# Performance work log

Hardware: AMD Instinct MI355X
Metric: run time of the kernel (lower is better)

Reference implementation:

```python
import jax, jax.numpy as jnp
import numpy as np
from jax import lax

B, C, H, W = 2, 512, 128, 128
HEADS = 4


def conv1x1(x, w):
    # x: [b,c,h,w], w: [o,c] (1x1 conv kernel squeezed)
    return jnp.einsum('bchw,oc->bohw', x, w)


def dwconv3x3(x, w):
    # depthwise 3x3, SAME padding; w: [c,1,3,3]
    return lax.conv_general_dilated(
        x, w, window_strides=(1, 1), padding='SAME',
        dimension_numbers=('NCHW', 'OIHW', 'NCHW'),
        feature_group_count=x.shape[1])


def l2norm(t):
    # F.normalize(dim=-1): x / max(||x||_2, eps)
    n = jnp.sqrt(jnp.sum(t * t, axis=-1, keepdims=True))
    return t / jnp.maximum(n, 1e-12)


def setup_inputs() -> dict:
    key = jax.random.key(0)
    ks = jax.random.split(key, 10)
    s = 0.02
    return {
        'x': jax.random.normal(ks[0], (B, C, H, W), jnp.float32),
        'y': jax.random.normal(ks[1], (B, C, H, W), jnp.float32),
        'temperature': jnp.ones((HEADS, 1, 1), jnp.float32),
        'q_w': s * jax.random.normal(ks[2], (C, C), jnp.float32),
        'q_dw': s * jax.random.normal(ks[3], (C, 1, 3, 3), jnp.float32),
        'kv_w': s * jax.random.normal(ks[4], (2 * C, C), jnp.float32),
        'kv_dw': s * jax.random.normal(ks[5], (2 * C, 1, 3, 3), jnp.float32),
        'proj_w': s * jax.random.normal(ks[6], (C, C), jnp.float32),
        'pos_embed': jnp.zeros((1, C, 1, 1), jnp.float32),
        'pos_q_w': s * jax.random.normal(ks[7], (C, C), jnp.float32),
        'pos_k_w': s * jax.random.normal(ks[8], (C, C), jnp.float32),
    }


def reference(x, y, temperature, q_w, q_dw, kv_w, kv_dw, proj_w, pos_embed, pos_q_w, pos_k_w):
    b, c, h, w = x.shape
    heads = temperature.shape[0]
    ch = c // heads

    def to_heads(t):  # [b,c,h,w] -> [b,head,ch,hw]
        return t.reshape(b, heads, ch, h * w)

    q = dwconv3x3(conv1x1(x, q_w), q_dw)
    kv = dwconv3x3(conv1x1(y, kv_w), kv_dw)
    k, v = jnp.split(kv, 2, axis=1)

    qh = l2norm(to_heads(q))
    kh = l2norm(to_heads(k))
    vh = to_heads(v)

    attn = jax.nn.softmax(jnp.einsum('bhcn,bhdn->bhcd', qh, kh) * temperature, axis=-1)
    out = jnp.einsum('bhcd,bhdn->bhcn', attn, vh)

    pos_x = x + pos_embed
    pq = to_heads(conv1x1(pos_x, pos_q_w))
    pk = to_heads(conv1x1(pos_x, pos_k_w))
    pos_attn = jax.nn.softmax(jnp.einsum('bhcn,bhdn->bhcd', pq, pk), axis=-1)
    pos_out = jnp.einsum('bhcd,bhdn->bhcn', pos_attn, vh)

    fused = (out + pos_out).reshape(b, c, h, w)
    return conv1x1(fused, proj_w)
```

## Files before the change

### kernel.cpp

```cpp
#include <hip/hip_runtime.h>


typedef _Float16 f16_t;
typedef __attribute__((ext_vector_type(8))) _Float16 f16x8;
typedef __attribute__((ext_vector_type(4))) float f32x4;

#define NDIM 16384

__device__ __forceinline__ void gload_lds16(const void* g, void* l) {
  __builtin_amdgcn_global_load_lds((__attribute__((address_space(1))) void*)g,
                                   (__attribute__((address_space(3))) void*)l, 16, 0, 0);
}

template<int EPI>
__device__ __forceinline__ void gemm_core_128(
    const f16_t* __restrict__ At, int lda,
    const f16_t* __restrict__ Bt, int ldb,
    void* __restrict__ Ct, int ldc, int K)
{
  __shared__ f16_t As[128 * 32];
  __shared__ f16_t Bs[128 * 32];
  const int tid = threadIdx.x;
  const int lane = tid & 63;
  const int wave = tid >> 6;
  const int wm = (wave >> 1) * 64;
  const int wn = (wave & 1) * 64;
  const int lr = lane & 15;
  const int lq = lane >> 4;

  const f16_t* gA0 = At + (size_t)(tid >> 2) * lda + (tid & 3) * 8;
  const f16_t* gA1 = At + (size_t)((tid + 256) >> 2) * lda + (tid & 3) * 8;
  const f16_t* gB0 = Bt + (size_t)(tid >> 2) * ldb + (tid & 3) * 8;
  const f16_t* gB1 = Bt + (size_t)((tid + 256) >> 2) * ldb + (tid & 3) * 8;
  f16_t* lA0 = &As[tid * 8];
  f16_t* lA1 = &As[(tid + 256) * 8];
  f16_t* lB0 = &Bs[tid * 8];
  f16_t* lB1 = &Bs[(tid + 256) * 8];

  f32x4 acc[4][4] = {};

  for (int kk = 0; kk < K; kk += 32) {
    if (kk) __syncthreads();
    gload_lds16(gA0 + kk, lA0);
    gload_lds16(gA1 + kk, lA1);
    gload_lds16(gB0 + kk, lB0);
    gload_lds16(gB1 + kk, lB1);
    __syncthreads();

    f16x8 af[4], bfr[4];
#pragma unroll
    for (int i = 0; i < 4; i++) {
      af[i]  = *(const f16x8*)&As[(wm + i * 16 + lr) * 32 + lq * 8];
      bfr[i] = *(const f16x8*)&Bs[(wn + i * 16 + lr) * 32 + lq * 8];
    }
#pragma unroll
    for (int i = 0; i < 4; i++)
#pragma unroll
      for (int j = 0; j < 4; j++)
        acc[i][j] = __builtin_amdgcn_mfma_f32_16x16x32_f16(af[i], bfr[j], acc[i][j], 0, 0, 0);
  }

#pragma unroll
  for (int i = 0; i < 4; i++)
#pragma unroll
    for (int j = 0; j < 4; j++)
#pragma unroll
      for (int r = 0; r < 4; r++) {
        int row = wm + i * 16 + lq * 4 + r;
        int col = wn + j * 16 + lr;
        float v = acc[i][j][r];
        if (EPI == 0)      ((f16_t*)Ct)[(size_t)row * ldc + col] = (f16_t)v;
        else if (EPI == 1) ((float*)Ct)[(size_t)row * ldc + col] = v;
        else               atomicAdd(&((float*)Ct)[(size_t)row * ldc + col], v);
      }
}

template<int EPI, typename CT>
__global__ __launch_bounds__(256) void gemm_bt_kernel(
    const f16_t* __restrict__ A, int lda, const f16_t* __restrict__ B, int ldb,
    CT* __restrict__ C, int ldc, int K)
{
  const f16_t* At = A + (size_t)blockIdx.y * 128 * lda;
  const f16_t* Bt = B + (size_t)blockIdx.x * 128 * ldb;
  CT* Ct = C + (size_t)blockIdx.y * 128 * ldc + (size_t)blockIdx.x * 128;
  gemm_core_128<EPI>(At, lda, Bt, ldb, (void*)Ct, ldc, K);
}

__global__ __launch_bounds__(256) void gram_kernel(
    const f16_t* __restrict__ xc, float* __restrict__ Gb)
{
  int ks = blockIdx.x, t = blockIdx.y;
  int ty = t >> 2, tx = t & 3;
  const f16_t* At = xc + (size_t)ty * 128 * NDIM + ks * 1024;
  const f16_t* Bt = xc + (size_t)tx * 128 * NDIM + ks * 1024;
  float* Ct = Gb + (size_t)ty * 128 * 512 + tx * 128;
  gemm_core_128<2>(At, NDIM, Bt, NDIM, Ct, 512, 1024);
}

__global__ __launch_bounds__(256) void qk_kernel(
    const f16_t* __restrict__ q, const f16_t* __restrict__ k,
    float* __restrict__ lgs_b)
{
  int ks = blockIdx.x, h = blockIdx.y;
  const f16_t* At = q + (size_t)h * 128 * NDIM + ks * 512;
  const f16_t* Bt = k + (size_t)h * 128 * NDIM + ks * 512;
  float* Ct = lgs_b + (size_t)h * 16384;
  gemm_core_128<2>(At, NDIM, Bt, NDIM, Ct, 128, 512);
}

__global__ __launch_bounds__(256) void transpose2_kernel(
    const float* __restrict__ sx, const float* __restrict__ sy,
    f16_t* __restrict__ dx, f16_t* __restrict__ dy)
{
  const float* src = blockIdx.z ? sy : sx;
  f16_t* dst = blockIdx.z ? dy : dx;
  __shared__ f16_t tile[32][33];
  int tx = threadIdx.x & 31, ty = threadIdx.x >> 5;
  int r0 = blockIdx.y * 32, c0 = blockIdx.x * 32;
#pragma unroll
  for (int k = 0; k < 4; k++) {
    int r = ty + k * 8;
    tile[r][tx] = (f16_t)src[(size_t)(r0 + r) * NDIM + c0 + tx];
  }
  __syncthreads();
#pragma unroll
  for (int k = 0; k < 4; k++) {
    int r = ty + k * 8;
    dst[(size_t)(c0 + r) * 512 + r0 + tx] = tile[tx][r];
  }
}

__global__ __launch_bounds__(256) void transpose_f16_kernel(
    const f16_t* __restrict__ src, f16_t* __restrict__ dst)
{
  __shared__ f16_t tile[32][33];
  int tx = threadIdx.x & 31, ty = threadIdx.x >> 5;
  int r0 = blockIdx.y * 32, c0 = blockIdx.x * 32;
#pragma unroll
  for (int k = 0; k < 4; k++) {
    int r = ty + k * 8;
    tile[r][tx] = src[(size_t)(r0 + r) * NDIM + c0 + tx];
  }
  __syncthreads();
#pragma unroll
  for (int k = 0; k < 4; k++) {
    int r = ty + k * 8;
    dst[(size_t)(c0 + r) * 512 + r0 + tx] = tile[tx][r];
  }
}

__global__ __launch_bounds__(256) void cast_x_kernel(
    const float* __restrict__ xb, f16_t* __restrict__ xc, float* __restrict__ srow_b)
{
  int c = blockIdx.y;
  int n = blockIdx.x * 256 + threadIdx.x;
  float v = xb[(size_t)c * NDIM + n];
  xc[(size_t)c * NDIM + n] = (f16_t)v;
  __shared__ float red[256];
  red[threadIdx.x] = v;
  __syncthreads();
  for (int s = 128; s > 0; s >>= 1) {
    if (threadIdx.x < s) red[threadIdx.x] += red[threadIdx.x + s];
    __syncthreads();
  }
  if (threadIdx.x == 0) atomicAdd(&srow_b[c], red[0]);
}

__global__ __launch_bounds__(256) void dwconv_kernel(
    const f16_t* __restrict__ in, const float* __restrict__ w,
    f16_t* __restrict__ outA, f16_t* __restrict__ outB,
    int splitC, float* __restrict__ norm2)
{
  const int c = blockIdx.y;
  const int t = threadIdx.x;
  const int xs = (t & 15) * 8;
  const int h0 = blockIdx.x * 64 + (t >> 4) * 4;
  const f16_t* src = in + (size_t)c * NDIM;
  const float* wc = w + c * 9;
  float w00 = wc[0], w01 = wc[1], w02 = wc[2];
  float w10 = wc[3], w11 = wc[4], w12 = wc[5];
  float w20 = wc[6], w21 = wc[7], w22 = wc[8];

  float rows[6][10];
#pragma unroll
  for (int i = 0; i < 6; i++) {
    int hh = h0 - 1 + i;
    int hc = hh < 0 ? 0 : (hh > 127 ? 127 : hh);
    f16x8 v = *(const f16x8*)(src + hc * 128 + xs);
    float l = __shfl_up((float)v[7], 1, 64);
    float r = __shfl_down((float)v[0], 1, 64);
    if ((t & 15) == 0) l = 0.f;
    if ((t & 15) == 15) r = 0.f;
    bool oob = (hh < 0) || (hh > 127);
    rows[i][0] = oob ? 0.f : l;
    rows[i][9] = oob ? 0.f : r;
#pragma unroll
    for (int j = 0; j < 8; j++) rows[i][1 + j] = oob ? 0.f : (float)v[j];
  }

  float s2 = 0.f;
  f16_t* dst = (c < splitC) ? outA + (size_t)c * NDIM
                            : outB + (size_t)(c - splitC) * NDIM;
#pragma unroll
  for (int i = 0; i < 4; i++) {
    f16x8 o;
#pragma unroll
    for (int j = 0; j < 8; j++) {
      float a = w00 * rows[i][j]     + w01 * rows[i][j + 1]     + w02 * rows[i][j + 2]
              + w10 * rows[i + 1][j] + w11 * rows[i + 1][j + 1] + w12 * rows[i + 1][j + 2]
              + w20 * rows[i + 2][j] + w21 * rows[i + 2][j + 1] + w22 * rows[i + 2][j + 2];
      o[j] = (f16_t)a;
      s2 += a * a;
    }
    *(f16x8*)(dst + (h0 + i) * 128 + xs) = o;
  }

  if (c < splitC) {
    __shared__ float red[256];
    red[t] = s2;
    __syncthreads();
    for (int s = 128; s > 0; s >>= 1) {
      if (t < s) red[t] += red[t + s];
      __syncthreads();
    }
    if (t == 0) atomicAdd(&norm2[c], red[0]);
  }
}

__global__ __launch_bounds__(64) void vec4_kernel(
    const float* __restrict__ pqw, const float* __restrict__ pkw,
    const float* __restrict__ pe, const float* __restrict__ srow_b,
    float* __restrict__ bq, float* __restrict__ bk,
    float* __restrict__ tq_b, float* __restrict__ tk_b)
{
  int o = blockIdx.x, which = blockIdx.y, lane = threadIdx.x;
  const float* w = ((which & 1) == 0) ? pqw + (size_t)o * 512 : pkw + (size_t)o * 512;
  const float* v = (which < 2) ? pe : srow_b;
  float s = 0.f;
  for (int c = lane; c < 512; c += 64) s += w[c] * v[c];
#pragma unroll
  for (int off = 32; off > 0; off >>= 1) s += __shfl_down(s, off, 64);
  if (lane == 0) {
    float* dst = (which == 0) ? bq : (which == 1) ? bk : (which == 2) ? tq_b : tk_b;
    dst[o] = s;
  }
}

__global__ __launch_bounds__(256) void posA_kernel(
    const float* __restrict__ pqw, const float* __restrict__ Gb,
    float* __restrict__ PqG)
{
  int tx = threadIdx.x & 15, ty = threadIdx.x >> 4;
  int h = blockIdx.z;
  int r = blockIdx.y * 16 + ty;
  int d = blockIdx.x * 16 + tx;
  const float* wr = pqw + (size_t)(h * 128 + r) * 512;
  float s = 0.f;
#pragma unroll 4
  for (int c = 0; c < 512; c++) s += wr[c] * Gb[(size_t)c * 512 + d];
  PqG[((size_t)h * 128 + r) * 512 + d] = s;
}

__global__ __launch_bounds__(256) void posB_kernel(
    const float* __restrict__ PqG, const float* __restrict__ pkw,
    const float* __restrict__ bq, const float* __restrict__ bk,
    const float* __restrict__ tq_b, const float* __restrict__ tk_b,
    float* __restrict__ lgp)
{
  int tx = threadIdx.x & 15, ty = threadIdx.x >> 4;
  int h = blockIdx.z;
  int r = blockIdx.y * 16 + ty;
  int s = blockIdx.x * 16 + tx;
  int gr = h * 128 + r, gs = h * 128 + s;
  const float* ar = PqG + (size_t)gr * 512;
  const float* kr = pkw + (size_t)gs * 512;
  float acc = 0.f;
#pragma unroll 4
  for (int c = 0; c < 512; c++) acc += ar[c] * kr[c];
  acc += tq_b[gr] * bk[gs] + bq[gr] * tk_b[gs] + 16384.f * bq[gr] * bk[gs];
  lgp[(size_t)h * 16384 + r * 128 + s] = acc;
}

__global__ __launch_bounds__(128) void smx_kernel(
    const float* __restrict__ lgs_b, const float* __restrict__ lgp,
    const float* __restrict__ n2q_b, const float* __restrict__ n2k_b,
    const float* __restrict__ temp, float* __restrict__ comb)
{
  int c = blockIdx.x & 127, h = blockIdx.x >> 7;
  int d = threadIdx.x;
  float rq = fmaxf(sqrtf(n2q_b[h * 128 + c]), 1e-12f);
  float rk = fmaxf(sqrtf(n2k_b[h * 128 + d]), 1e-12f);
  float s0 = lgs_b[(size_t)h * 16384 + c * 128 + d] / (rq * rk) * temp[h];
  float s1 = lgp[(size_t)h * 16384 + c * 128 + d];
  __shared__ float sh[128];
  sh[d] = s0; __syncthreads();
  for (int s = 64; s > 0; s >>= 1) { if (d < s) sh[d] = fmaxf(sh[d], sh[d + s]); __syncthreads(); }
  float m0 = sh[0]; __syncthreads();
  float e0 = __expf(s0 - m0);
  sh[d] = e0; __syncthreads();
  for (int s = 64; s > 0; s >>= 1) { if (d < s) sh[d] += sh[d + s]; __syncthreads(); }
  float z0 = sh[0]; __syncthreads();
  sh[d] = s1; __syncthreads();
  for (int s = 64; s > 0; s >>= 1) { if (d < s) sh[d] = fmaxf(sh[d], sh[d + s]); __syncthreads(); }
  float m1 = sh[0]; __syncthreads();
  float e1 = __expf(s1 - m1);
  sh[d] = e1; __syncthreads();
  for (int s = 64; s > 0; s >>= 1) { if (d < s) sh[d] += sh[d + s]; __syncthreads(); }
  float z1 = sh[0];
  comb[(size_t)h * 16384 + c * 128 + d] = e0 / z0 + e1 / z1;
}

__global__ __launch_bounds__(256) void mb_kernel(
    const float* __restrict__ proj_w, const float* __restrict__ comb,
    f16_t* __restrict__ Mb)
{
  int tx = threadIdx.x & 15, ty = threadIdx.x >> 4;
  int h = blockIdx.z;
  int o = blockIdx.y * 16 + ty;
  int d = blockIdx.x * 16 + tx;
  const float* pw = proj_w + (size_t)o * 512 + h * 128;
  const float* cm = comb + (size_t)h * 16384 + d;
  float s = 0.f;
#pragma unroll 4
  for (int r = 0; r < 128; r++) s += pw[r] * cm[(size_t)r * 128];
  Mb[(size_t)o * 512 + h * 128 + d] = (f16_t)s;
}

__global__ __launch_bounds__(256) void castw_kernel(
    const float* __restrict__ q_w, const float* __restrict__ kv_w,
    f16_t* __restrict__ Wq, f16_t* __restrict__ Wkv)
{
  int i = blockIdx.x * 256 + threadIdx.x;
  if (i < 262144) Wq[i] = (f16_t)q_w[i];
  else Wkv[i - 262144] = (f16_t)kv_w[i - 262144];
}

__global__ __launch_bounds__(256) void zero_kernel(float* __restrict__ p, long n) {
  long i = (long)blockIdx.x * 256 + threadIdx.x;
  if (i < n) p[i] = 0.f;
}

extern "C" void kernel_launch(void* const* d_in, const int* in_sizes, int n_in,
                              void* d_out, int out_size, void* d_ws, size_t ws_size,
                              hipStream_t stream) {
  const float* x      = (const float*)d_in[0];
  const float* y      = (const float*)d_in[1];
  const float* temp   = (const float*)d_in[2];
  const float* q_w    = (const float*)d_in[3];
  const float* q_dw   = (const float*)d_in[4];
  const float* kv_w   = (const float*)d_in[5];
  const float* kv_dw  = (const float*)d_in[6];
  const float* proj_w = (const float*)d_in[7];
  const float* pe     = (const float*)d_in[8];
  const float* pqw    = (const float*)d_in[9];
  const float* pkw    = (const float*)d_in[10];

  const size_t MB = 1ull << 20;
  const size_t N = NDIM;
  char* Wb = (char*)d_ws;
  f16_t* Abuf = (f16_t*)(Wb);
  f16_t* Bbuf = (f16_t*)(Wb + 16 * MB);
  f16_t* Cbuf = (f16_t*)(Wb + 32 * MB);
  f16_t* Dbuf = (f16_t*)(Wb + 48 * MB);
  char* SM = Wb + 64 * MB;
  float* G    = (float*)(SM);
  float* lgs  = (float*)(SM + 2 * MB);
  float* n2q  = (float*)(SM + 2 * MB + 512 * 1024);
  float* n2k  = n2q + 1024;
  float* srow = n2k + 1024;
  float* bq   = (float*)(SM + 3 * MB);
  float* bk   = bq + 512;
  float* tq   = bk + 512;
  float* tk   = tq + 1024;
  f16_t* Wq   = (f16_t*)(SM + 3 * MB + 16 * 1024);
  f16_t* Wkv  = (f16_t*)(SM + 3 * MB + 16 * 1024 + 512 * 1024);
  float* PqG  = (float*)(SM + 5 * MB);
  float* lgp  = (float*)(SM + 6 * MB);
  float* comb = (float*)(SM + 6 * MB + 256 * 1024);
  f16_t* Mb   = (f16_t*)(SM + 6 * MB + 512 * 1024);

  zero_kernel<<<2572, 256, 0, stream>>>((float*)SM, 658432L);
  castw_kernel<<<3072, 256, 0, stream>>>(q_w, kv_w, Wq, Wkv);

  for (int b = 0; b < 2; b++) {
    const float* xb = x + (size_t)b * 512 * N;
    const float* yb = y + (size_t)b * 512 * N;
    float* srow_b = srow + b * 512;
    float* Gb = G + (size_t)b * 512 * 512;
    float* lgs_b = lgs + (size_t)b * 4 * 16384;
    f16_t* kvp = (f16_t*)d_out + (size_t)b * 1024 * N;
    float* outb = (float*)d_out + (size_t)b * 512 * N;

    cast_x_kernel<<<dim3(64, 512), 256, 0, stream>>>(xb, Abuf, srow_b);
    vec4_kernel<<<dim3(512, 4), 64, 0, stream>>>(pqw, pkw, pe, srow_b,
                                                 bq, bk, tq + b * 512, tk + b * 512);
    gram_kernel<<<dim3(16, 16), 256, 0, stream>>>(Abuf, Gb);
    transpose2_kernel<<<dim3(512, 16, 2), 256, 0, stream>>>(xb, yb, Bbuf, Cbuf);
    gemm_bt_kernel<0, f16_t><<<dim3(128, 4), 256, 0, stream>>>(
        Wq, 512, Bbuf, 512, Dbuf, (int)N, 512);
    gemm_bt_kernel<0, f16_t><<<dim3(128, 8), 256, 0, stream>>>(
        Wkv, 512, Cbuf, 512, kvp, (int)N, 512);
    dwconv_kernel<<<dim3(2, 512), 256, 0, stream>>>(
        Dbuf, q_dw, Abuf, (f16_t*)nullptr, 512, n2q + b * 512);
    dwconv_kernel<<<dim3(2, 1024), 256, 0, stream>>>(
        kvp, kv_dw, Dbuf, Cbuf, 512, n2k + b * 512);
    transpose_f16_kernel<<<dim3(512, 16), 256, 0, stream>>>(Cbuf, Bbuf);
    qk_kernel<<<dim3(32, 4), 256, 0, stream>>>(Abuf, Dbuf, lgs_b);
    posA_kernel<<<dim3(32, 8, 4), 256, 0, stream>>>(pqw, Gb, PqG);
    posB_kernel<<<dim3(8, 8, 4), 256, 0, stream>>>(PqG, pkw, bq, bk,
                                                   tq + b * 512, tk + b * 512, lgp);
    smx_kernel<<<512, 128, 0, stream>>>(lgs_b, lgp, n2q + b * 512, n2k + b * 512,
                                        temp, comb);
    mb_kernel<<<dim3(8, 32, 4), 256, 0, stream>>>(proj_w, comb, Mb);
    gemm_bt_kernel<1, float><<<dim3(128, 4), 256, 0, stream>>>(
        Mb, 512, Bbuf, 512, outb, (int)N, 512);
  }

  (void)in_sizes; (void)n_in; (void)out_size; (void)ws_size;
}
```

Measured before the change: 797.3 us.

## Vectorize transposes and cast, use wave-shuffle reductions in cast, dwconv, softmax

The transpose kernels now use 64x64 tiles with 16-byte vector loads and 8-wide f16 vector stores in place of scalar element accesses. The cast kernel handles 8 elements per thread with vector loads and stores. Cast, dwconv and softmax replace LDS tree reductions and their many barriers with wave shuffle reductions. The softmax block shrinks to one wave handling two elements per thread. The aim is to cut memory instruction count and synchronisation overhead in these bandwidth-bound helper kernels, at the risk of LDS bank conflicts in the column reads of the transpose.

After: 658.9 us. -17.4%, faster.

```diff
diff --git a/kernel.cpp b/kernel.cpp
--- a/kernel.cpp
+++ b/kernel.cpp
@@ -2,6 +2,7 @@
 
 
 typedef _Float16 f16_t;
+typedef __attribute__((ext_vector_type(4))) _Float16 f16x4;
 typedef __attribute__((ext_vector_type(8))) _Float16 f16x8;
 typedef __attribute__((ext_vector_type(4))) float f32x4;
 
@@ -114,56 +115,80 @@
 {
   const float* src = blockIdx.z ? sy : sx;
   f16_t* dst = blockIdx.z ? dy : dx;
-  __shared__ f16_t tile[32][33];
-  int tx = threadIdx.x & 31, ty = threadIdx.x >> 5;
-  int r0 = blockIdx.y * 32, c0 = blockIdx.x * 32;
-#pragma unroll
-  for (int k = 0; k < 4; k++) {
-    int r = ty + k * 8;
-    tile[r][tx] = (f16_t)src[(size_t)(r0 + r) * NDIM + c0 + tx];
+  __shared__ f16_t tile[64][72];
+  const int t = threadIdx.x;
+  const int r0 = blockIdx.y * 64, c0 = blockIdx.x * 64;
+  {
+    int tx = t & 15, ty = t >> 4;
+#pragma unroll
+    for (int k = 0; k < 4; k++) {
+      int r = ty + k * 16;
+      f32x4 v = *(const f32x4*)(src + (size_t)(r0 + r) * NDIM + c0 + tx * 4);
+      f16x4 o = { (f16_t)v[0], (f16_t)v[1], (f16_t)v[2], (f16_t)v[3] };
+      *(f16x4*)&tile[r][tx * 4] = o;
+    }
   }
   __syncthreads();
-#pragma unroll
-  for (int k = 0; k < 4; k++) {
-    int r = ty + k * 8;
-    dst[(size_t)(c0 + r) * 512 + r0 + tx] = tile[tx][r];
+  {
+    int j0 = t >> 3, cg = (t & 7) * 8;
+#pragma unroll
+    for (int k = 0; k < 2; k++) {
+      int j = j0 + k * 32;
+      f16x8 o;
+#pragma unroll
+      for (int i = 0; i < 8; i++) o[i] = tile[cg + i][j];
+      *(f16x8*)(dst + (size_t)(c0 + j) * 512 + r0 + cg) = o;
+    }
   }
 }
 
 __global__ __launch_bounds__(256) void transpose_f16_kernel(
     const f16_t* __restrict__ src, f16_t* __restrict__ dst)
 {
-  __shared__ f16_t tile[32][33];
-  int tx = threadIdx.x & 31, ty = threadIdx.x >> 5;
-  int r0 = blockIdx.y * 32, c0 = blockIdx.x * 32;
-#pragma unroll
-  for (int k = 0; k < 4; k++) {
-    int r = ty + k * 8;
-    tile[r][tx] = src[(size_t)(r0 + r) * NDIM + c0 + tx];
+  __shared__ f16_t tile[64][72];
+  const int t = threadIdx.x;
+  const int r0 = blockIdx.y * 64, c0 = blockIdx.x * 64;
+  {
+    int tx = t & 7, ty = t >> 3;
+#pragma unroll
+    for (int k = 0; k < 2; k++) {
+      int r = ty + k * 32;
+      f16x8 v = *(const f16x8*)(src + (size_t)(r0 + r) * NDIM + c0 + tx * 8);
+      *(f16x8*)&tile[r][tx * 8] = v;
+    }
   }
   __syncthreads();
-#pragma unroll
-  for (int k = 0; k < 4; k++) {
-    int r = ty + k * 8;
-    dst[(size_t)(c0 + r) * 512 + r0 + tx] = tile[tx][r];
+  {
+    int j0 = t >> 3, cg = (t & 7) * 8;
+#pragma unroll
+    for (int k = 0; k < 2; k++) {
+      int j = j0 + k * 32;
+      f16x8 o;
+#pragma unroll
+      for (int i = 0; i < 8; i++) o[i] = tile[cg + i][j];
+      *(f16x8*)(dst + (size_t)(c0 + j) * 512 + r0 + cg) = o;
+    }
   }
 }
 
 __global__ __launch_bounds__(256) void cast_x_kernel(
     const float* __restrict__ xb, f16_t* __restrict__ xc, float* __restrict__ srow_b)
 {
-  int c = blockIdx.y;
-  int n = blockIdx.x * 256 + threadIdx.x;
-  float v = xb[(size_t)c * NDIM + n];
-  xc[(size_t)c * NDIM + n] = (f16_t)v;
-  __shared__ float red[256];
-  red[threadIdx.x] = v;
+  const int c = blockIdx.y;
+  const int base = blockIdx.x * 2048 + threadIdx.x * 8;
+  const float* src = xb + (size_t)c * NDIM + base;
+  f32x4 a = *(const f32x4*)src;
+  f32x4 b = *(const f32x4*)(src + 4);
+  f16x8 o = { (f16_t)a[0], (f16_t)a[1], (f16_t)a[2], (f16_t)a[3],
+              (f16_t)b[0], (f16_t)b[1], (f16_t)b[2], (f16_t)b[3] };
+  *(f16x8*)(xc + (size_t)c * NDIM + base) = o;
+  float s = a[0] + a[1] + a[2] + a[3] + b[0] + b[1] + b[2] + b[3];
+#pragma unroll
+  for (int off = 32; off > 0; off >>= 1) s += __shfl_down(s, off, 64);
+  __shared__ float ws[4];
+  if ((threadIdx.x & 63) == 0) ws[threadIdx.x >> 6] = s;
   __syncthreads();
-  for (int s = 128; s > 0; s >>= 1) {
-    if (threadIdx.x < s) red[threadIdx.x] += red[threadIdx.x + s];
-    __syncthreads();
-  }
-  if (threadIdx.x == 0) atomicAdd(&srow_b[c], red[0]);
+  if (threadIdx.x == 0) atomicAdd(&srow_b[c], ws[0] + ws[1] + ws[2] + ws[3]);
 }
 
 __global__ __launch_bounds__(256) void dwconv_kernel(
@@ -216,14 +241,12 @@
   }
 
   if (c < splitC) {
-    __shared__ float red[256];
-    red[t] = s2;
+#pragma unroll
+    for (int off = 32; off > 0; off >>= 1) s2 += __shfl_down(s2, off, 64);
+    __shared__ float ws[4];
+    if ((t & 63) == 0) ws[t >> 6] = s2;
     __syncthreads();
-    for (int s = 128; s > 0; s >>= 1) {
-      if (t < s) red[t] += red[t + s];
-      __syncthreads();
-    }
-    if (t == 0) atomicAdd(&norm2[c], red[0]);
+    if (t == 0) atomicAdd(&norm2[c], ws[0] + ws[1] + ws[2] + ws[3]);
   }
 }
 
@@ -281,33 +304,42 @@
   lgp[(size_t)h * 16384 + r * 128 + s] = acc;
 }
 
-__global__ __launch_bounds__(128) void smx_kernel(
+__global__ __launch_bounds__(64) void smx_kernel(
     const float* __restrict__ lgs_b, const float* __restrict__ lgp,
     const float* __restrict__ n2q_b, const float* __restrict__ n2k_b,
     const float* __restrict__ temp, float* __restrict__ comb)
 {
   int c = blockIdx.x & 127, h = blockIdx.x >> 7;
-  int d = threadIdx.x;
+  int l = threadIdx.x;
+  int d0 = l, d1 = l + 64;
   float rq = fmaxf(sqrtf(n2q_b[h * 128 + c]), 1e-12f);
-  float rk = fmaxf(sqrtf(n2k_b[h * 128 + d]), 1e-12f);
-  float s0 = lgs_b[(size_t)h * 16384 + c * 128 + d] / (rq * rk) * temp[h];
-  float s1 = lgp[(size_t)h * 16384 + c * 128 + d];
-  __shared__ float sh[128];
-  sh[d] = s0; __syncthreads();
-  for (int s = 64; s > 0; s >>= 1) { if (d < s) sh[d] = fmaxf(sh[d], sh[d + s]); __syncthreads(); }
-  float m0 = sh[0]; __syncthreads();
-  float e0 = __expf(s0 - m0);
-  sh[d] = e0; __syncthreads();
-  for (int s = 64; s > 0; s >>= 1) { if (d < s) sh[d] += sh[d + s]; __syncthreads(); }
-  float z0 = sh[0]; __syncthreads();
-  sh[d] = s1; __syncthreads();
-  for (int s = 64; s > 0; s >>= 1) { if (d < s) sh[d] = fmaxf(sh[d], sh[d + s]); __syncthreads(); }
-  float m1 = sh[0]; __syncthreads();
-  float e1 = __expf(s1 - m1);
-  sh[d] = e1; __syncthreads();
-  for (int s = 64; s > 0; s >>= 1) { if (d < s) sh[d] += sh[d + s]; __syncthreads(); }
-  float z1 = sh[0];
-  comb[(size_t)h * 16384 + c * 128 + d] = e0 / z0 + e1 / z1;
+  float rk0 = fmaxf(sqrtf(n2k_b[h * 128 + d0]), 1e-12f);
+  float rk1 = fmaxf(sqrtf(n2k_b[h * 128 + d1]), 1e-12f);
+  float t = temp[h];
+  size_t base = (size_t)h * 16384 + c * 128;
+  float s00 = lgs_b[base + d0] / (rq * rk0) * t;
+  float s01 = lgs_b[base + d1] / (rq * rk1) * t;
+  float s10 = lgp[base + d0];
+  float s11 = lgp[base + d1];
+
+  float m0 = fmaxf(s00, s01);
+#pragma unroll
+  for (int msk = 32; msk > 0; msk >>= 1) m0 = fmaxf(m0, __shfl_xor(m0, msk, 64));
+  float e00 = __expf(s00 - m0), e01 = __expf(s01 - m0);
+  float z0 = e00 + e01;
+#pragma unroll
+  for (int msk = 32; msk > 0; msk >>= 1) z0 += __shfl_xor(z0, msk, 64);
+
+  float m1 = fmaxf(s10, s11);
+#pragma unroll
+  for (int msk = 32; msk > 0; msk >>= 1) m1 = fmaxf(m1, __shfl_xor(m1, msk, 64));
+  float e10 = __expf(s10 - m1), e11 = __expf(s11 - m1);
+  float z1 = e10 + e11;
+#pragma unroll
+  for (int msk = 32; msk > 0; msk >>= 1) z1 += __shfl_xor(z1, msk, 64);
+
+  comb[base + d0] = e00 / z0 + e10 / z1;
+  comb[base + d1] = e01 / z0 + e11 / z1;
 }
 
 __global__ __launch_bounds__(256) void mb_kernel(
@@ -391,11 +423,11 @@
     f16_t* kvp = (f16_t*)d_out + (size_t)b * 1024 * N;
     float* outb = (float*)d_out + (size_t)b * 512 * N;
 
-    cast_x_kernel<<<dim3(64, 512), 256, 0, stream>>>(xb, Abuf, srow_b);
+    cast_x_kernel<<<dim3(8, 512), 256, 0, stream>>>(xb, Abuf, srow_b);
     vec4_kernel<<<dim3(512, 4), 64, 0, stream>>>(pqw, pkw, pe, srow_b,
                                                  bq, bk, tq + b * 512, tk + b * 512);
     gram_kernel<<<dim3(16, 16), 256, 0, stream>>>(Abuf, Gb);
-    transpose2_kernel<<<dim3(512, 16, 2), 256, 0, stream>>>(xb, yb, Bbuf, Cbuf);
+    transpose2_kernel<<<dim3(256, 8, 2), 256, 0, stream>>>(xb, yb, Bbuf, Cbuf);
     gemm_bt_kernel<0, f16_t><<<dim3(128, 4), 256, 0, stream>>>(
         Wq, 512, Bbuf, 512, Dbuf, (int)N, 512);
     gemm_bt_kernel<0, f16_t><<<dim3(128, 8), 256, 0, stream>>>(
@@ -404,13 +436,13 @@
         Dbuf, q_dw, Abuf, (f16_t*)nullptr, 512, n2q + b * 512);
     dwconv_kernel<<<dim3(2, 1024), 256, 0, stream>>>(
         kvp, kv_dw, Dbuf, Cbuf, 512, n2k + b * 512);
-    transpose_f16_kernel<<<dim3(512, 16), 256, 0, stream>>>(Cbuf, Bbuf);
+    transpose_f16_kernel<<<dim3(256, 8), 256, 0, stream>>>(Cbuf, Bbuf);
     qk_kernel<<<dim3(32, 4), 256, 0, stream>>>(Abuf, Dbuf, lgs_b);
     posA_kernel<<<dim3(32, 8, 4), 256, 0, stream>>>(pqw, Gb, PqG);
     posB_kernel<<<dim3(8, 8, 4), 256, 0, stream>>>(PqG, pkw, bq, bk,
                                                    tq + b * 512, tk + b * 512, lgp);
-    smx_kernel<<<512, 128, 0, stream>>>(lgs_b, lgp, n2q + b * 512, n2k + b * 512,
-                                        temp, comb);
+    smx_kernel<<<512, 64, 0, stream>>>(lgs_b, lgp, n2q + b * 512, n2k + b * 512,
+                                       temp, comb);
     mb_kernel<<<dim3(8, 32, 4), 256, 0, stream>>>(proj_w, comb, Mb);
     gemm_bt_kernel<1, float><<<dim3(128, 4), 256, 0, stream>>>(
         Mb, 512, Bbuf, 512, outb, (int)N, 512);
```
